# Performance work log

Hardware: AMD Instinct MI355X
Metric: run time of the kernel (lower is better)

The kernel has to match this reference:

```python
import jax, jax.numpy as jnp
import numpy as np
from jax import lax


def _leaky(x):
    # LeakyReLU, negative_slope=0.1
    return jnp.where(x > 0, x, 0.1 * x)


def _conv(x, w, pad, groups=1):
    # NCHW / OIHW 2D conv, stride 1
    return lax.conv_general_dilated(
        x, w, (1, 1), [(pad, pad), (pad, pad)],
        dimension_numbers=("NCHW", "OIHW", "NCHW"),
        feature_group_count=groups)


def setup_inputs() -> dict:
    key = jax.random.key(0)
    ks = jax.random.split(key, 12)
    B, C, H, W = 16, 64, 256, 256
    KS = 3

    def nrm(k, shape, fan_in):
        return jax.random.normal(k, shape, jnp.float32) / np.float32(np.sqrt(fan_in))

    return {
        "x": jax.random.normal(ks[0], (B, C, H, W), jnp.float32),
        "t": jax.random.normal(ks[1], (B, 1, 1, 1), jnp.float32),
        # t_process: 1x1 convs (1->64, 64->64), no bias -> stored as matrices
        "tW1": nrm(ks[2], (C, 1), 1),
        "tW2": nrm(ks[3], (C, C), C),
        # f_process: two 3x3 convs 64->64 with bias
        "fW1": nrm(ks[4], (C, C, KS, KS), C * KS * KS),
        "fb1": jnp.zeros((C,), jnp.float32),
        "fW2": nrm(ks[5], (C, C, KS, KS), C * KS * KS),
        "fb2": jnp.zeros((C,), jnp.float32),
        # kernel branch: 1x1 convs (1->64, 64->64*9), no bias
        "kW1": nrm(ks[6], (C, 1), 1),
        "kW2": nrm(ks[7], (C * KS * KS, C), C),
        # conv33: 3x3 conv 64->64 with bias
        "cW": nrm(ks[8], (C, C, KS, KS), C * KS * KS),
        "cb": jnp.zeros((C,), jnp.float32),
    }


def reference(x, t, tW1, tW2, fW1, fb1, fW2, fb2, kW1, kW2, cW, cb):
    b, c, h, w = x.shape
    KS = 3

    # f_process: Conv3x3 -> LeakyReLU -> Conv3x3 -> LeakyReLU
    f = _leaky(_conv(x, fW1, 1) + fb1[None, :, None, None])
    f = _leaky(_conv(f, fW2, 1) + fb2[None, :, None, None])

    # t is (b,1,1,1); 1x1 convs on it are per-sample matmuls
    ts = t.reshape(b, 1)
    # t_process: Conv1x1 -> LeakyReLU -> Conv1x1 -> Sigmoid -> (b,c,1,1)
    mv = jax.nn.sigmoid(_leaky(ts @ tW1.T) @ tW2.T).reshape(b, c, 1, 1)

    # kernel branch: Conv1x1 -> LeakyReLU -> Conv1x1 -> LeakyReLU -> (b*c,1,3,3)
    kern = _leaky(_leaky(ts @ kW1.T) @ kW2.T).reshape(b * c, 1, KS, KS)

    # per-sample-channel dynamic depthwise conv: groups = b*c
    out = _conv(f.reshape(1, b * c, h, w), kern, (KS - 1) // 2,
                groups=b * c).reshape(b, c, h, w)

    # modulation gating + residual 3x3 conv
    return out * mv + _conv(x, cW, 1) + cb[None, :, None, None]
```

## Files before the change

### kernel.cpp

```cpp
#include <hip/hip_runtime.h>
#include <cstdint>

using short8  = __attribute__((ext_vector_type(8))) short;
using short4v = __attribute__((ext_vector_type(4))) short;
using f32x16  = __attribute__((ext_vector_type(16))) float;
using float4v = __attribute__((ext_vector_type(4))) float;
typedef unsigned short ushort_t;

#define CHUNK_ROW 520
#define CHUNK_SLOTS 1560
#define BUF_SLOTS 1632
#define XSHW (BUF_SLOTS * 8)
#define WSHW (20 * 512)
#define XB0 WSHW
#define XB1 (WSHW + XSHW)
#define DYN1 ((WSHW + 2 * XSHW) * 2)
#define WSHM (40 * 512)
#define XBM WSHM
#define DYN02 ((WSHM + XSHW) * 2)

__device__ __forceinline__ float lrelu(float x) { return x > 0.f ? x : 0.1f * x; }

__device__ __forceinline__ ushort_t f2bf(float f) {
    union { float f; unsigned u; } v; v.f = f;
    unsigned r = (v.u + 0x7FFFu + ((v.u >> 16) & 1u)) >> 16;
    return (ushort_t)r;
}
__device__ __forceinline__ float bf2f(ushort_t b) {
    union { unsigned u; float f; } v; v.u = ((unsigned)b) << 16; return v.f;
}

__device__ __forceinline__ void gload_lds16(const ushort_t* g, ushort_t* l) {
    __builtin_amdgcn_global_load_lds(
        (const __attribute__((address_space(1))) void*)g,
        (__attribute__((address_space(3))) void*)l, 16, 0, 0);
}

#define VMCNT(n) asm volatile("s_waitcnt vmcnt(" #n ")" ::: "memory")
#define RBAR() __builtin_amdgcn_s_barrier()
#define SCHED0() __builtin_amdgcn_sched_barrier(0)

__global__ void k_tiny(const float* __restrict__ t, const float* __restrict__ tW1,
                       const float* __restrict__ tW2, const float* __restrict__ kW1,
                       const float* __restrict__ kW2, float* __restrict__ ktr) {
    int b = blockIdx.x;
    int c = threadIdx.x;
    __shared__ float h1[64], g1[64];
    float ts = t[b];
    h1[c] = lrelu(ts * tW1[c]);
    g1[c] = lrelu(ts * kW1[c]);
    __syncthreads();
    float s = 0.f;
    for (int j = 0; j < 64; ++j) s = fmaf(tW2[c * 64 + j], h1[j], s);
    float mvv = 1.f / (1.f + expf(-s));
    for (int q = 0; q < 9; ++q) {
        float s2 = 0.f;
        for (int j = 0; j < 64; ++j) s2 = fmaf(kW2[(c * 9 + q) * 64 + j], g1[j], s2);
        ktr[b * 576 + q * 64 + c] = lrelu(s2) * mvv;
    }
}

__global__ void k_zrow(ushort_t* __restrict__ z) {
    int i = blockIdx.x * 256 + threadIdx.x;
    *(short8*)(z + (size_t)i * 8) = (short8)0;
}

__global__ void k_pack(const float* __restrict__ w1, const float* __restrict__ w2,
                       const float* __restrict__ w3, ushort_t* __restrict__ wpM,
                       ushort_t* __restrict__ wp2) {
    int idx = blockIdx.x * 256 + threadIdx.x;
    const int NM = 4 * 36 * 512;
    if (idx >= NM + 4 * 18 * 512) return;
    const float* W;
    ushort_t* dst;
    int chunk, row, e;
    if (idx < NM) {
        chunk = idx / (36 * 512);
        int rem = idx % (36 * 512);
        row = rem / 512;
        e = rem % 512;
        W = (row < 18) ? w1 : w3;
        dst = wpM + idx;
        row %= 18;
    } else {
        int i2 = idx - NM;
        chunk = i2 / (18 * 512);
        int rem = i2 % (18 * 512);
        row = rem / 512;
        e = rem % 512;
        W = w2;
        dst = wp2 + i2;
    }
    int lane = e >> 3, j = e & 7;
    int t = row >> 1, ct = row & 1;
    int co = ct * 32 + (lane & 31);
    int ci = chunk * 16 + (lane >> 5) * 8 + j;
    *dst = f2bf(W[(co * 64 + ci) * 9 + t]);
}

__global__ __launch_bounds__(256) void k_tr(const float* __restrict__ x,
                                            ushort_t* __restrict__ xbf) {
    int bid = blockIdx.x;
    int h = bid & 255, b = bid >> 8;
    int t = threadIdx.x;
    for (int it = 0; it < 8; ++it) {
        int idx = t + it * 256;
        int g = idx & 7, w = idx >> 3;
        const float* src = x + (((size_t)(b * 64 + g * 8) * 256 + h) * 256 + w);
        short8 v;
#pragma unroll
        for (int j = 0; j < 8; ++j) v[j] = (short)f2bf(src[(size_t)j * 65536]);
        *(short8*)(xbf + (((size_t)(b * 256 + h) * 256 + w) * 64 + g * 8)) = v;
    }
}

#define STAGE_X(chunk, xbase)                                                    \
    {                                                                            \
        _Pragma("unroll")                                                        \
        for (int i_ = 0; i_ < 7; ++i_) {                                         \
            int base_ = wv * 390 + i_ * 64;                                      \
            int S_ = base_ + lane;                                               \
            S_ = S_ < CHUNK_SLOTS ? S_ : CHUNK_SLOTS - 1;                        \
            int row_ = (S_ >= 2 * CHUNK_ROW) ? 2 : (S_ >= CHUNK_ROW ? 1 : 0);    \
            int rem_ = S_ - row_ * CHUNK_ROW;                                    \
            int mg_ = rem_ >> 3, sl_ = rem_ & 7;                                 \
            int sp_ = sl_ ^ (mg_ & 7);                                           \
            int p_ = mg_ * 4 + (sp_ >> 1), g_ = sp_ & 1;                         \
            int wsx_ = p_ - 1;                                                   \
            bool edge_ = (unsigned)wsx_ >= 256u;                                 \
            const ushort_t* rp_ = (row_ == 0) ? rb0 : (row_ == 1 ? rb1 : rb2);   \
            const ushort_t* src_ =                                               \
                edge_ ? zv : (rp_ + wsx_ * 64 + (chunk)*16 + g_ * 8);            \
            gload_lds16(src_, xs + (xbase) + (size_t)base_ * 8);                 \
        }                                                                        \
    }

#define STAGE_W(chunk)                                                           \
    {                                                                            \
        _Pragma("unroll")                                                        \
        for (int i_ = 0; i_ < 5; ++i_) {                                         \
            int row_ = wv * 5 + i_;                                              \
            int rc_ = row_ > 17 ? 17 : row_;                                     \
            gload_lds16(wp + (size_t)((chunk)*18 + rc_) * 512 + lane * 8,        \
                        xs + (size_t)row_ * 512);                                \
        }                                                                        \
    }

#define STAGE_WM(chunk)                                                          \
    {                                                                            \
        _Pragma("unroll")                                                        \
        for (int i_ = 0; i_ < 10; ++i_) {                                        \
            int row_ = wv * 10 + i_;                                             \
            int rc_ = row_ > 35 ? 35 : row_;                                     \
            gload_lds16(wpM + (size_t)((chunk)*36 + rc_) * 512 + lane * 8,       \
                        xs + (size_t)row_ * 512);                                \
        }                                                                        \
    }

#define COMPUTE(xbase)                                                           \
    {                                                                            \
        __builtin_amdgcn_s_setprio(1);                                           \
        _Pragma("unroll")                                                        \
        for (int t_ = 0; t_ < 9; ++t_) {                                         \
            short8 a0 = *(const short8*)(xs + (size_t)(t_ * 2) * 512 + lane * 8);\
            short8 a1 = *(const short8*)(xs + (size_t)(t_ * 2 + 1) * 512 + lane * 8); \
            const int dwx_ = t_ % 3, rr_ = t_ / 3;                               \
            _Pragma("unroll")                                                    \
            for (int pt_ = 0; pt_ < 2; ++pt_) {                                  \
                int p_ = pw0 + pt_ * 32 + l31 + dwx_;                            \
                int mg_ = p_ >> 2;                                               \
                int sl_ = ((p_ & 3) * 2 + lhi) ^ (mg_ & 7);                      \
                short8 bf = *(const short8*)(                                    \
                    xs + (xbase) + (size_t)(rr_ * CHUNK_ROW + mg_ * 8 + sl_) * 8);\
                acc[0][pt_] = __builtin_amdgcn_mfma_f32_32x32x16_bf16(           \
                    a0, bf, acc[0][pt_], 0, 0, 0);                               \
                acc[1][pt_] = __builtin_amdgcn_mfma_f32_32x32x16_bf16(           \
                    a1, bf, acc[1][pt_], 0, 0, 0);                               \
            }                                                                    \
        }                                                                        \
        __builtin_amdgcn_s_setprio(0);                                           \
    }

#define COMPUTE_M()                                                              \
    {                                                                            \
        __builtin_amdgcn_s_setprio(1);                                           \
        _Pragma("unroll")                                                        \
        for (int t_ = 0; t_ < 9; ++t_) {                                         \
            short8 a0 = *(const short8*)(xs + (size_t)(t_ * 2) * 512 + lane * 8);\
            short8 a1 = *(const short8*)(xs + (size_t)(t_ * 2 + 1) * 512 + lane * 8); \
            short8 c0 = *(const short8*)(xs + (size_t)(18 + t_ * 2) * 512 + lane * 8); \
            short8 c1 = *(const short8*)(xs + (size_t)(19 + t_ * 2) * 512 + lane * 8); \
            const int dwx_ = t_ % 3, rr_ = t_ / 3;                               \
            _Pragma("unroll")                                                    \
            for (int pt_ = 0; pt_ < 2; ++pt_) {                                  \
                int p_ = pw0 + pt_ * 32 + l31 + dwx_;                            \
                int mg_ = p_ >> 2;                                               \
                int sl_ = ((p_ & 3) * 2 + lhi) ^ (mg_ & 7);                      \
                short8 bf = *(const short8*)(                                    \
                    xs + XBM + (size_t)(rr_ * CHUNK_ROW + mg_ * 8 + sl_) * 8);   \
                accA[0][pt_] = __builtin_amdgcn_mfma_f32_32x32x16_bf16(          \
                    a0, bf, accA[0][pt_], 0, 0, 0);                              \
                accA[1][pt_] = __builtin_amdgcn_mfma_f32_32x32x16_bf16(          \
                    a1, bf, accA[1][pt_], 0, 0, 0);                              \
                accC[0][pt_] = __builtin_amdgcn_mfma_f32_32x32x16_bf16(          \
                    c0, bf, accC[0][pt_], 0, 0, 0);                              \
                accC[1][pt_] = __builtin_amdgcn_mfma_f32_32x32x16_bf16(          \
                    c1, bf, accC[1][pt_], 0, 0, 0);                              \
            }                                                                    \
        }                                                                        \
        __builtin_amdgcn_s_setprio(0);                                           \
    }

__global__ __launch_bounds__(256, 2) void k_conv02(
    const ushort_t* __restrict__ in, const ushort_t* __restrict__ zv,
    const ushort_t* __restrict__ wpM, const float* __restrict__ ba,
    const float* __restrict__ bc, ushort_t* __restrict__ f1out,
    float* __restrict__ cres) {
    extern __shared__ __align__(16) ushort_t xs[];
    const int tid = threadIdx.x;
    const int lane = tid & 63;
    const int wv = tid >> 6;
    const unsigned bid = blockIdx.x;
    const unsigned L = (bid & 7u) * 512u + (bid >> 3);
    const int h = L & 255, b = L >> 8;
    const int l31 = lane & 31, lhi = lane >> 5;
    const int pw0 = wv * 64;

    const ushort_t* rb0 = (h > 0)   ? in + ((size_t)(b * 256 + h - 1)) * 16384 : zv;
    const ushort_t* rb1 =             in + ((size_t)(b * 256 + h)) * 16384;
    const ushort_t* rb2 = (h < 255) ? in + ((size_t)(b * 256 + h + 1)) * 16384 : zv;

    f32x16 accA[2][2], accC[2][2];
#pragma unroll
    for (int a = 0; a < 2; ++a)
#pragma unroll
        for (int c = 0; c < 2; ++c) { accA[a][c] = (f32x16)0.0f; accC[a][c] = (f32x16)0.0f; }

#pragma unroll
    for (int ch = 0; ch < 4; ++ch) {
        STAGE_WM(ch);
        STAGE_X(ch, XBM);
        VMCNT(0);
        RBAR(); SCHED0();
        COMPUTE_M();
        RBAR();
    }

    const int co_b = 4 * lhi;
    {
        ushort_t* outb = f1out + ((size_t)(b * 256 + h)) * 16384;
#pragma unroll
        for (int ct = 0; ct < 2; ++ct)
#pragma unroll
            for (int pt = 0; pt < 2; ++pt) {
                int pix = pw0 + pt * 32 + l31;
                ushort_t* po = outb + (size_t)pix * 64 + ct * 32 + co_b;
#pragma unroll
                for (int q = 0; q < 4; ++q) {
                    float4v bv = *(const float4v*)(ba + ct * 32 + co_b + 8 * q);
                    short4v sv;
#pragma unroll
                    for (int m = 0; m < 4; ++m) {
                        float v = lrelu(accA[ct][pt][q * 4 + m] + bv[m]);
                        sv[m] = (short)f2bf(v);
                    }
                    *(short4v*)(po + 8 * q) = sv;
                }
            }
    }
    {
        float* pb = cres + (((size_t)b * 64) << 16) + h * 256;
#pragma unroll
        for (int ct = 0; ct < 2; ++ct)
#pragma unroll
            for (int pt = 0; pt < 2; ++pt) {
                int pix = pw0 + pt * 32 + l31;
#pragma unroll
                for (int q = 0; q < 4; ++q) {
                    float4v bv = *(const float4v*)(bc + ct * 32 + co_b + 8 * q);
#pragma unroll
                    for (int m = 0; m < 4; ++m) {
                        int c = ct * 32 + co_b + 8 * q + m;
                        pb[((size_t)c << 16) + pix] = accC[ct][pt][q * 4 + m] + bv[m];
                    }
                }
            }
    }
}

__global__ __launch_bounds__(256, 2) void k_conv1(
    const ushort_t* __restrict__ in, const ushort_t* __restrict__ zv,
    const ushort_t* __restrict__ wp, const float* __restrict__ bias,
    ushort_t* __restrict__ outp) {
    extern __shared__ __align__(16) ushort_t xs[];
    const int tid = threadIdx.x;
    const int lane = tid & 63;
    const int wv = tid >> 6;
    const unsigned bid = blockIdx.x;
    const unsigned L = (bid & 7u) * 512u + (bid >> 3);
    const int h = L & 255, b = L >> 8;
    const int l31 = lane & 31, lhi = lane >> 5;
    const int pw0 = wv * 64;

    const ushort_t* rb0 = (h > 0)   ? in + ((size_t)(b * 256 + h - 1)) * 16384 : zv;
    const ushort_t* rb1 =             in + ((size_t)(b * 256 + h)) * 16384;
    const ushort_t* rb2 = (h < 255) ? in + ((size_t)(b * 256 + h + 1)) * 16384 : zv;

    f32x16 acc[2][2];
#pragma unroll
    for (int a = 0; a < 2; ++a)
#pragma unroll
        for (int c = 0; c < 2; ++c) acc[a][c] = (f32x16)0.0f;

    STAGE_W(0);
    STAGE_X(0, XB0);
    STAGE_X(1, XB1);
    VMCNT(7);
    RBAR(); SCHED0();
    COMPUTE(XB0);
    RBAR();
    STAGE_W(1); STAGE_X(2, XB0);
    VMCNT(7);
    RBAR(); SCHED0();
    COMPUTE(XB1);
    RBAR();
    STAGE_W(2); STAGE_X(3, XB1);
    VMCNT(7);
    RBAR(); SCHED0();
    COMPUTE(XB0);
    RBAR();
    STAGE_W(3);
    VMCNT(0);
    RBAR(); SCHED0();
    COMPUTE(XB1);

    const int co_b = 4 * lhi;
    ushort_t* pb = outp + (((size_t)b * 64) << 16) + h * 256;
#pragma unroll
    for (int ct = 0; ct < 2; ++ct)
#pragma unroll
        for (int pt = 0; pt < 2; ++pt) {
            int pix = pw0 + pt * 32 + l31;
#pragma unroll
            for (int q = 0; q < 4; ++q) {
                float4v bv = *(const float4v*)(bias + ct * 32 + co_b + 8 * q);
#pragma unroll
                for (int m = 0; m < 4; ++m) {
                    int c = ct * 32 + co_b + 8 * q + m;
                    float v = lrelu(acc[ct][pt][q * 4 + m] + bv[m]);
                    pb[((size_t)c << 16) + pix] = f2bf(v);
                }
            }
        }
}

__global__ __launch_bounds__(256) void k_fin(const ushort_t* __restrict__ f2,
                                             const float* __restrict__ ktr,
                                             float* __restrict__ out) {
    __shared__ __align__(16) ushort_t s[10 * 272];
    const unsigned bid = blockIdx.x;
    const unsigned L = (bid & 7u) * 4096u + (bid >> 3);
    const int hb = L & 31, c = (L >> 5) & 63, b = L >> 11;
    const int h0 = hb * 8;
    const int w = threadIdx.x;

    const ushort_t* f2c = f2 + (((size_t)(b * 64 + c)) << 16);
    for (int i = w; i < 320; i += 256) {
        int r = i >> 5, seg = i & 31;
        int hs = h0 - 1 + r;
        short8 v = (short8)0;
        if ((unsigned)hs < 256u) v = *(const short8*)(f2c + hs * 256 + seg * 8);
        *(short8*)(&s[r * 272 + 8 + seg * 8]) = v;
        if (seg == 0) s[r * 272 + 7] = 0;
        if (seg == 31) s[r * 272 + 264] = 0;
    }
    __syncthreads();

    float kv[9];
#pragma unroll
    for (int t9 = 0; t9 < 9; ++t9) kv[t9] = ktr[b * 576 + t9 * 64 + c];

    float lv[10], cv[10], rv[10];
#pragma unroll
    for (int r = 0; r < 10; ++r) {
        lv[r] = bf2f(s[r * 272 + 7 + w]);
        cv[r] = bf2f(s[r * 272 + 8 + w]);
        rv[r] = bf2f(s[r * 272 + 9 + w]);
    }

    float* ob = out + (((size_t)(b * 64 + c)) << 16) + h0 * 256 + w;
#pragma unroll
    for (int rr = 0; rr < 8; ++rr) {
        float dwv = 0.f;
#pragma unroll
        for (int r3 = 0; r3 < 3; ++r3) {
            dwv = fmaf(kv[r3 * 3 + 0], lv[rr + r3], dwv);
            dwv = fmaf(kv[r3 * 3 + 1], cv[rr + r3], dwv);
            dwv = fmaf(kv[r3 * 3 + 2], rv[rr + r3], dwv);
        }
        float* po = ob + rr * 256;
        *po = *po + dwv;
    }
}

extern "C" void kernel_launch(void* const* d_in, const int* in_sizes, int n_in,
                              void* d_out, int out_size, void* d_ws, size_t ws_size,
                              hipStream_t stream) {
    const float* x   = (const float*)d_in[0];
    const float* t   = (const float*)d_in[1];
    const float* tW1 = (const float*)d_in[2];
    const float* tW2 = (const float*)d_in[3];
    const float* fW1 = (const float*)d_in[4];
    const float* fb1 = (const float*)d_in[5];
    const float* fW2 = (const float*)d_in[6];
    const float* fb2 = (const float*)d_in[7];
    const float* kW1 = (const float*)d_in[8];
    const float* kW2 = (const float*)d_in[9];
    const float* cW  = (const float*)d_in[10];
    const float* cb  = (const float*)d_in[11];

    char* ws = (char*)d_ws;
    float*    ktr  = (float*)ws;
    ushort_t* wpM  = (ushort_t*)(ws + 65536);
    ushort_t* wp2  = wpM + 4 * 36 * 512;
    ushort_t* zv   = (ushort_t*)(ws + 294912);
    ushort_t* xbf  = (ushort_t*)(ws + (512u << 10));
    ushort_t* f1bf = (ushort_t*)(ws + (512u << 10) + ((size_t)128 << 20));
    ushort_t* f2n  = xbf;
    float*    out  = (float*)d_out;

    hipFuncSetAttribute(reinterpret_cast<const void*>(&k_conv02),
                        hipFuncAttributeMaxDynamicSharedMemorySize, DYN02);
    hipFuncSetAttribute(reinterpret_cast<const void*>(&k_conv1),
                        hipFuncAttributeMaxDynamicSharedMemorySize, DYN1);

    k_tiny<<<dim3(16), dim3(64), 0, stream>>>(t, tW1, tW2, kW1, kW2, ktr);
    k_zrow<<<dim3(8), dim3(256), 0, stream>>>(zv);
    k_pack<<<dim3((4 * 36 * 512 + 4 * 18 * 512 + 255) / 256), dim3(256), 0, stream>>>(
        fW1, fW2, cW, wpM, wp2);
    k_tr<<<dim3(4096), dim3(256), 0, stream>>>(x, xbf);

    k_conv02<<<dim3(4096), dim3(256), DYN02, stream>>>(
        xbf, zv, wpM, fb1, cb, f1bf, out);
    k_conv1<<<dim3(4096), dim3(256), DYN1, stream>>>(f1bf, zv, wp2, fb2, f2n);
    k_fin<<<dim3(32768), dim3(256), 0, stream>>>(f2n, ktr, out);
}
```

Before: 586.7 us.

## Single-buffer conv1 LDS for higher occupancy; coalesce NCHW-to-NHWC transpose via LDS

The first conv kernel drops its double-buffered input staging, using one LDS buffer with a full wait before each chunk's compute, and raises launch bounds to three blocks per CU. This trades the overlap of global loads with MFMA compute for more resident waves to hide latency. Separately, the input transpose kernel now reads coalesced rows of width 64 into a padded shared tile before writing channel-packed bf16 vectors, replacing strided per-channel global reads.

```diff
diff --git a/kernel.cpp b/kernel.cpp
--- a/kernel.cpp
+++ b/kernel.cpp
@@ -13,8 +13,7 @@
 #define XSHW (BUF_SLOTS * 8)
 #define WSHW (20 * 512)
 #define XB0 WSHW
-#define XB1 (WSHW + XSHW)
-#define DYN1 ((WSHW + 2 * XSHW) * 2)
+#define DYN1 ((WSHW + XSHW) * 2)
 #define WSHM (40 * 512)
 #define XBM WSHM
 #define DYN02 ((WSHM + XSHW) * 2)
@@ -100,17 +99,30 @@
 
 __global__ __launch_bounds__(256) void k_tr(const float* __restrict__ x,
                                             ushort_t* __restrict__ xbf) {
+    __shared__ ushort_t tl[64][66];
     int bid = blockIdx.x;
     int h = bid & 255, b = bid >> 8;
     int t = threadIdx.x;
-    for (int it = 0; it < 8; ++it) {
-        int idx = t + it * 256;
-        int g = idx & 7, w = idx >> 3;
-        const float* src = x + (((size_t)(b * 64 + g * 8) * 256 + h) * 256 + w);
-        short8 v;
-#pragma unroll
-        for (int j = 0; j < 8; ++j) v[j] = (short)f2bf(src[(size_t)j * 65536]);
-        *(short8*)(xbf + (((size_t)(b * 256 + h) * 256 + w) * 64 + g * 8)) = v;
+    int cb = t >> 6;
+    int wl = t & 63;
+    for (int wt = 0; wt < 4; ++wt) {
+        __syncthreads();
+#pragma unroll
+        for (int cc = 0; cc < 16; ++cc) {
+            int c = cc * 4 + cb;
+            float v = x[(((size_t)(b * 64 + c)) << 16) + h * 256 + wt * 64 + wl];
+            tl[c][wl] = f2bf(v);
+        }
+        __syncthreads();
+        int g = t & 7, w2 = t >> 3;
+#pragma unroll
+        for (int half = 0; half < 2; ++half) {
+            int w = w2 + half * 32;
+            short8 v;
+#pragma unroll
+            for (int j = 0; j < 8; ++j) v[j] = (short)tl[g * 8 + j][w];
+            *(short8*)(xbf + (((size_t)(b * 256 + h) * 256 + wt * 64 + w) * 64 + g * 8)) = v;
+        }
     }
 }
 
@@ -288,7 +300,7 @@
     }
 }
 
-__global__ __launch_bounds__(256, 2) void k_conv1(
+__global__ __launch_bounds__(256, 3) void k_conv1(
     const ushort_t* __restrict__ in, const ushort_t* __restrict__ zv,
     const ushort_t* __restrict__ wp, const float* __restrict__ bias,
     ushort_t* __restrict__ outp) {
@@ -312,27 +324,15 @@
 #pragma unroll
         for (int c = 0; c < 2; ++c) acc[a][c] = (f32x16)0.0f;
 
-    STAGE_W(0);
-    STAGE_X(0, XB0);
-    STAGE_X(1, XB1);
-    VMCNT(7);
-    RBAR(); SCHED0();
-    COMPUTE(XB0);
-    RBAR();
-    STAGE_W(1); STAGE_X(2, XB0);
-    VMCNT(7);
-    RBAR(); SCHED0();
-    COMPUTE(XB1);
-    RBAR();
-    STAGE_W(2); STAGE_X(3, XB1);
-    VMCNT(7);
-    RBAR(); SCHED0();
-    COMPUTE(XB0);
-    RBAR();
-    STAGE_W(3);
-    VMCNT(0);
-    RBAR(); SCHED0();
-    COMPUTE(XB1);
+#pragma unroll
+    for (int ch = 0; ch < 4; ++ch) {
+        STAGE_W(ch);
+        STAGE_X(ch, XB0);
+        VMCNT(0);
+        RBAR(); SCHED0();
+        COMPUTE(XB0);
+        RBAR();
+    }
 
     const int co_b = 4 * lhi;
     ushort_t* pb = outp + (((size_t)b * 64) << 16) + h * 256;
```

Measured after the change: 601.2 us. 1.02x slower.
